# Kernel tuning notes

Hardware: AMD Instinct MI355X
Metric: run time of the kernel (lower is better)

## Reference

```python
import jax, jax.numpy as jnp
import numpy as np

N_HEADS = 16
N_KV_HEADS = 4
ROPE_BASE = 10000.0


def rotate_half(x):
    d = x.shape[-1] // 2
    return jnp.concatenate((-x[..., d:], x[..., :d]), axis=-1)


def rope_cos_sin(seq_len, head_dim, dtype):
    inv_freq = 1.0 / (ROPE_BASE ** (jnp.arange(0, head_dim, 2, dtype=jnp.float32) / head_dim))
    t = jnp.arange(seq_len, dtype=jnp.float32)
    freqs = jnp.outer(t, inv_freq)            # [S, d/2]
    emb = jnp.concatenate((freqs, freqs), axis=-1)  # [S, d]
    return emb.astype(dtype), None  # placeholder; cos/sin computed by caller


def setup_inputs() -> dict:
    key = jax.random.key(0)
    ks = jax.random.split(key, 5)
    B, S, H = 1, 2048, 2048
    kv_dim = (H // N_HEADS) * N_KV_HEADS  # 512
    scale = 1.0 / np.sqrt(H)
    return {
        "hidden_states": jax.random.normal(ks[0], (B, S, H), dtype=jnp.float32),
        "Wq": jax.random.normal(ks[1], (H, H), dtype=jnp.float32) * scale,
        "Wk": jax.random.normal(ks[2], (kv_dim, H), dtype=jnp.float32) * scale,
        "Wv": jax.random.normal(ks[3], (kv_dim, H), dtype=jnp.float32) * scale,
        "Wo": jax.random.normal(ks[4], (H, H), dtype=jnp.float32) * scale,
    }


def reference(hidden_states, Wq, Wk, Wv, Wo):
    B, S, H = hidden_states.shape
    nH, nKV = N_HEADS, N_KV_HEADS
    d = H // nH
    groups = nH // nKV

    # projections (nn.Linear: y = x @ W.T)
    q = (hidden_states @ Wq.T).reshape(B, S, nH, d)   # [B,S,nH,d]
    k = (hidden_states @ Wk.T).reshape(B, S, nKV, d)  # [B,S,nKV,d]
    v = (hidden_states @ Wv.T).reshape(B, S, nKV, d)

    # RoPE
    inv_freq = 1.0 / (ROPE_BASE ** (jnp.arange(0, d, 2, dtype=jnp.float32) / d))
    freqs = jnp.outer(jnp.arange(S, dtype=jnp.float32), inv_freq)  # [S,d/2]
    emb = jnp.concatenate((freqs, freqs), axis=-1)                 # [S,d]
    cos = jnp.cos(emb)[None, :, None, :]
    sin = jnp.sin(emb)[None, :, None, :]
    q = q * cos + rotate_half(q) * sin
    k = k * cos + rotate_half(k) * sin

    # GQA: repeat_interleave kv heads over head axis
    k = jnp.repeat(k, groups, axis=2)  # [B,S,nH,d]
    v = jnp.repeat(v, groups, axis=2)

    # causal scaled dot-product attention
    scores = jnp.einsum('bqhd,bkhd->bhqk', q, k) / jnp.sqrt(jnp.asarray(d, q.dtype))
    causal = jnp.tril(jnp.ones((S, S), dtype=bool))
    scores = jnp.where(causal[None, None], scores, jnp.asarray(-jnp.inf, scores.dtype))
    probs = jax.nn.softmax(scores, axis=-1)
    out = jnp.einsum('bhqk,bkhd->bqhd', probs, v)  # [B,S,nH,d]
    out = out.reshape(B, S, H) @ Wo.T
    return out
```

## Files before the change

kernel.cpp:

```cpp
#include <hip/hip_runtime.h>
#include <cstdint>
#include <cstddef>


typedef __bf16 bf16_t;
typedef bf16_t bf16x4_t __attribute__((ext_vector_type(4)));
typedef bf16_t bf16x8_t __attribute__((ext_vector_type(8)));
typedef float f32x4_t __attribute__((ext_vector_type(4)));

__device__ __forceinline__ void async_copy16(void* lds_base, const void* gsrc) {
  auto g = reinterpret_cast<__attribute__((address_space(1))) void*>(
      reinterpret_cast<uintptr_t>(gsrc));
  auto l = reinterpret_cast<__attribute__((address_space(3))) void*>(
      static_cast<uint32_t>(reinterpret_cast<uintptr_t>(lds_base)));
  __builtin_amdgcn_global_load_lds(g, l, 16, 0, 0);
}

__global__ __launch_bounds__(256) void cvt_all(const float* __restrict__ hs,
                                               const float* __restrict__ wq,
                                               const float* __restrict__ wk,
                                               const float* __restrict__ wv,
                                               const float* __restrict__ wo,
                                               bf16_t* __restrict__ regA,
                                               bf16_t* __restrict__ regB,
                                               bf16_t* __restrict__ regWo) {
  const int b = blockIdx.x;
  const float* src;
  bf16_t* dst;
  int rel;
  if (b < 2048) { src = hs; dst = regA; rel = b; }
  else if (b < 4096) { src = wq; dst = regB; rel = b - 2048; }
  else if (b < 4608) { src = wk; dst = regB + 4194304; rel = b - 4096; }
  else if (b < 5120) { src = wv; dst = regB + 5242880; rel = b - 4608; }
  else { src = wo; dst = regWo; rel = b - 5120; }
  const int i = (rel * 256 + threadIdx.x) * 8;
  float4 v0 = *(const float4*)(src + i);
  float4 v1 = *(const float4*)(src + i + 4);
  bf16x8_t o = {(bf16_t)v0.x, (bf16_t)v0.y, (bf16_t)v0.z, (bf16_t)v0.w,
                (bf16_t)v1.x, (bf16_t)v1.y, (bf16_t)v1.z, (bf16_t)v1.w};
  *(bf16x8_t*)(dst + i) = o;
}

template <typename OutT, bool ROPE>
__global__ __launch_bounds__(256) void gemm_bt64(const bf16_t* __restrict__ A,
                                                 const bf16_t* __restrict__ B,
                                                 OutT* __restrict__ C,
                                                 int M, int N, int K) {
  __shared__ bf16_t As[64 * 64];
  __shared__ bf16_t Bs[128 * 64];
  const int tid = threadIdx.x;
  const int lane = tid & 63;
  const int quad = lane >> 4;
  const int l15 = lane & 15;
  const int l7 = l15 & 7;
  const int wave = tid >> 6;
  const int bm = blockIdx.x * 64;
  const int bn = blockIdx.y * 128;
  const int wm = (wave >> 1) * 32;
  const int wn32 = (wave & 1) * 32;
  const int coff[4] = {wn32, wn32 + 16, wn32 + 64, wn32 + 80};

  f32x4_t acc[2][4] = {};

  for (int k0 = 0; k0 < K; k0 += 64) {
#pragma unroll
    for (int it = 0; it < 2; ++it) {
      const int slot = it * 256 + tid;
      const int r = slot >> 3;
      const int q = (slot & 7) ^ (r & 7);
      const int wbase = it * 2048 + (tid & 192) * 8;
      async_copy16(As + wbase, A + (size_t)(bm + r) * K + k0 + q * 8);
    }
#pragma unroll
    for (int it = 0; it < 4; ++it) {
      const int slot = it * 256 + tid;
      const int r = slot >> 3;
      const int q = (slot & 7) ^ (r & 7);
      const int wbase = it * 2048 + (tid & 192) * 8;
      async_copy16(Bs + wbase, B + (size_t)(bn + r) * K + k0 + q * 8);
    }
    __syncthreads();
#pragma unroll
    for (int kk = 0; kk < 64; kk += 32) {
      const int kc = kk >> 3;
      bf16x8_t af[2], bfv[4];
#pragma unroll
      for (int i = 0; i < 2; ++i)
        af[i] = *(const bf16x8_t*)(As + (wm + i * 16 + l15) * 64 +
                                   (((kc + quad) ^ l7) * 8));
#pragma unroll
      for (int i = 0; i < 4; ++i)
        bfv[i] = *(const bf16x8_t*)(Bs + (coff[i] + l15) * 64 +
                                    (((kc + quad) ^ l7) * 8));
#pragma unroll
      for (int mi = 0; mi < 2; ++mi)
#pragma unroll
        for (int ni = 0; ni < 4; ++ni)
          acc[mi][ni] = __builtin_amdgcn_mfma_f32_16x16x32_bf16(
              af[mi], bfv[ni], acc[mi][ni], 0, 0, 0);
    }
    __syncthreads();
  }

  if (ROPE && bn < 2560) {
#pragma unroll
    for (int pair = 0; pair < 2; ++pair) {
      const int i_d = wn32 + pair * 16 + l15;
      const float inv = exp2f(-(float)i_d * 0.20762050593045702f);
#pragma unroll
      for (int mi = 0; mi < 2; ++mi) {
#pragma unroll
        for (int r = 0; r < 4; ++r) {
          const int s_row = bm + wm + mi * 16 + quad * 4 + r;
          float sn, cs;
          sincosf((float)s_row * inv, &sn, &cs);
          const float x0 = acc[mi][pair][r];
          const float x1 = acc[mi][pair + 2][r];
          acc[mi][pair][r] = x0 * cs - x1 * sn;
          acc[mi][pair + 2][r] = x1 * cs + x0 * sn;
        }
      }
    }
  }

#pragma unroll
  for (int mi = 0; mi < 2; ++mi) {
#pragma unroll
    for (int r = 0; r < 4; ++r) {
      const int row = bm + wm + mi * 16 + quad * 4 + r;
#pragma unroll
      for (int ni = 0; ni < 4; ++ni)
        C[(size_t)row * N + bn + coff[ni] + l15] = (OutT)acc[mi][ni][r];
    }
  }
}

__global__ __launch_bounds__(256) void attn_kernel(
    const bf16_t* __restrict__ qkv, float* __restrict__ Op,
    float* __restrict__ lp) {
  __shared__ bf16_t Ks[64 * 128];
  __shared__ bf16_t Vt[128 * 64];
  __shared__ bf16_t Ps[4 * 16 * 64];
  const int tid = threadIdx.x;
  const int lane = tid & 63;
  const int wave = tid >> 6;
  const int quad = lane >> 4;
  const int l15 = lane & 15;
  const int l7 = l15 & 7;
  const int j = blockIdx.x;
  const int half = j >> 9;
  const int j2 = j & 511;
  const int qb = (j2 < 256) ? (31 - (j2 >> 4)) : ((j2 - 256) >> 4);
  const int h = j2 & 15;
  const int kvh = h >> 2;
  const int nh0 = (qb + 2) >> 1;
  const int kbS = half ? nh0 : 0;
  const int kbE = half ? (qb + 1) : nh0;
  const float scale = 0.08838834764831845f;

  const int rk0 = tid >> 4;
  const int cq = tid & 15;
  const int dv2 = lane * 2;

  bf16x8_t qf[4];
  {
    const bf16_t* qbase =
        qkv + (size_t)(qb * 64 + wave * 16 + l15) * 3072 + h * 128 + quad * 8;
#pragma unroll
    for (int kf = 0; kf < 4; ++kf) qf[kf] = *(const bf16x8_t*)(qbase + kf * 32);
  }

  f32x4_t o[8] = {};
  float lsum[4] = {0.f, 0.f, 0.f, 0.f};

  bf16x8_t kreg[4];
  uint32_t vbuf[2][8];
  auto load_tile = [&](int kb) {
    const bf16_t* kbase = qkv + (size_t)(kb * 64) * 3072 + 2048 + kvh * 128;
    const bf16_t* vbase = qkv + (size_t)(kb * 64) * 3072 + 2560 + kvh * 128;
#pragma unroll
    for (int it = 0; it < 4; ++it)
      kreg[it] =
          *(const bf16x8_t*)(kbase + (size_t)(it * 16 + rk0) * 3072 + cq * 8);
#pragma unroll
    for (int it = 0; it < 2; ++it) {
      const int kg8 = it * 4 + wave;
#pragma unroll
      for (int t = 0; t < 8; ++t)
        vbuf[it][t] =
            *(const uint32_t*)(vbase + (size_t)(kg8 * 8 + t) * 3072 + dv2);
    }
  };

  if (kbS < kbE) {
    load_tile(kbS);

    for (int kb = kbS; kb < kbE; ++kb) {
      __syncthreads();
#pragma unroll
      for (int it = 0; it < 4; ++it)
        *(bf16x8_t*)(Ks + (it * 16 + rk0) * 128 + ((cq ^ rk0) * 8)) = kreg[it];
#pragma unroll
      for (int it = 0; it < 2; ++it) {
        const int kg8 = it * 4 + wave;
        bf16x8_t lov, hiv;
#pragma unroll
        for (int t = 0; t < 8; ++t) {
          const uint32_t u = vbuf[it][t];
          lov[t] = __builtin_bit_cast(bf16_t, (unsigned short)(u & 0xffff));
          hiv[t] = __builtin_bit_cast(bf16_t, (unsigned short)(u >> 16));
        }
        *(bf16x8_t*)(Vt + (size_t)dv2 * 64 + ((kg8 ^ (dv2 & 7)) * 8)) = lov;
        *(bf16x8_t*)(Vt + (size_t)(dv2 + 1) * 64 +
                     ((kg8 ^ ((dv2 + 1) & 7)) * 8)) = hiv;
      }
      __syncthreads();
      if (kb + 1 < kbE) load_tile(kb + 1);

      f32x4_t sc[4] = {};
#pragma unroll
      for (int kf = 0; kf < 4; ++kf) {
#pragma unroll
        for (int ni = 0; ni < 4; ++ni) {
          bf16x8_t bfr = *(const bf16x8_t*)(Ks + (ni * 16 + l15) * 128 +
                                            (((kf * 4 + quad) ^ l15) * 8));
          sc[ni] = __builtin_amdgcn_mfma_f32_16x16x32_bf16(qf[kf], bfr, sc[ni],
                                                           0, 0, 0);
        }
      }

      float p[4][4];
#pragma unroll
      for (int r = 0; r < 4; ++r) {
        const int sq = qb * 64 + wave * 16 + quad * 4 + r;
#pragma unroll
        for (int ni = 0; ni < 4; ++ni) {
          float arg = fmaf(sc[ni][r], scale, -16.0f);
          if (kb == qb && (kb * 64 + ni * 16 + l15) > sq) arg = -100.0f;
          const float e = __expf(arg);
          p[ni][r] = e;
          lsum[r] += e;
        }
      }

      bf16_t* pw = Ps + wave * 16 * 64;
#pragma unroll
      for (int ni = 0; ni < 4; ++ni)
#pragma unroll
        for (int r = 0; r < 4; ++r) {
          const int prow = quad * 4 + r;
          pw[prow * 64 + (((ni * 2 + (l15 >> 3)) ^ (prow & 7)) * 8) + l7] =
              (bf16_t)p[ni][r];
        }

#pragma unroll
      for (int kf = 0; kf < 2; ++kf) {
        bf16x8_t af =
            *(const bf16x8_t*)(pw + l15 * 64 + (((kf * 4 + quad) ^ l7) * 8));
#pragma unroll
        for (int ni = 0; ni < 8; ++ni) {
          bf16x8_t bfr = *(const bf16x8_t*)(Vt + (ni * 16 + l15) * 64 +
                                            (((kf * 4 + quad) ^ l7) * 8));
          o[ni] =
              __builtin_amdgcn_mfma_f32_16x16x32_bf16(af, bfr, o[ni], 0, 0, 0);
        }
      }
    }
  }

#pragma unroll
  for (int m = 1; m <= 8; m <<= 1)
#pragma unroll
    for (int r = 0; r < 4; ++r) lsum[r] += __shfl_xor(lsum[r], m, 64);

  float* obase = Op + (size_t)half * 4194304 +
                 (size_t)(qb * 64 + wave * 16 + quad * 4) * 2048 + h * 128 + l15;
#pragma unroll
  for (int r = 0; r < 4; ++r) {
#pragma unroll
    for (int ni = 0; ni < 8; ++ni)
      obase[(size_t)r * 2048 + ni * 16] = o[ni][r];
    if (l15 == 0) {
      const int row = qb * 64 + wave * 16 + quad * 4 + r;
      lp[(half * 2048 + row) * 16 + h] = lsum[r];
    }
  }
}

__global__ __launch_bounds__(256) void combine_kernel(
    const float* __restrict__ Op, const float* __restrict__ lp,
    bf16_t* __restrict__ out) {
  const int idx = (blockIdx.x * 256 + threadIdx.x) * 8;
  const int s = idx >> 11;
  const int col = idx & 2047;
  const int h = col >> 7;
  const float l = lp[s * 16 + h] + lp[(2048 + s) * 16 + h];
  const float inv = 1.0f / l;
  const float* pa = Op + (size_t)s * 2048 + col;
  const float* pb = pa + 4194304;
  float4 a0 = *(const float4*)(pa);
  float4 a1 = *(const float4*)(pa + 4);
  float4 b0 = *(const float4*)(pb);
  float4 b1 = *(const float4*)(pb + 4);
  bf16x8_t o = {(bf16_t)((a0.x + b0.x) * inv), (bf16_t)((a0.y + b0.y) * inv),
                (bf16_t)((a0.z + b0.z) * inv), (bf16_t)((a0.w + b0.w) * inv),
                (bf16_t)((a1.x + b1.x) * inv), (bf16_t)((a1.y + b1.y) * inv),
                (bf16_t)((a1.z + b1.z) * inv), (bf16_t)((a1.w + b1.w) * inv)};
  *(bf16x8_t*)(out + idx) = o;
}

extern "C" void kernel_launch(void* const* d_in, const int* in_sizes, int n_in,
                              void* d_out, int out_size, void* d_ws, size_t ws_size,
                              hipStream_t stream) {
  const float* hidden = (const float*)d_in[0];
  const float* Wq = (const float*)d_in[1];
  const float* Wk = (const float*)d_in[2];
  const float* Wv = (const float*)d_in[3];
  const float* Wo = (const float*)d_in[4];

  char* ws = (char*)d_ws;
  bf16_t* regA = (bf16_t*)ws;
  bf16_t* regB = (bf16_t*)(ws + (size_t)(8u << 20));
  float* Opart = (float*)(ws + (size_t)(8u << 20));
  bf16_t* regC = (bf16_t*)(ws + (size_t)(40u << 20));
  bf16_t* regWo = (bf16_t*)(ws + (size_t)(53u << 20));
  float* lpart = (float*)(ws + (size_t)(61u << 20));

  cvt_all<<<7168, 256, 0, stream>>>(hidden, Wq, Wk, Wv, Wo, regA, regB, regWo);

  gemm_bt64<bf16_t, true><<<dim3(32, 24), 256, 0, stream>>>(regA, regB, regC,
                                                            2048, 3072, 2048);

  attn_kernel<<<1024, 256, 0, stream>>>(regC, Opart, lpart);

  combine_kernel<<<2048, 256, 0, stream>>>(Opart, lpart, regA);

  gemm_bt64<float, false><<<dim3(32, 16), 256, 0, stream>>>(
      regA, regWo, (float*)d_out, 2048, 2048, 2048);
}
```

Before: 218.0 us.

## Split attention KV range into variable segments per query block and reduce with atomics

```diff
diff --git a/kernel.cpp b/kernel.cpp
--- a/kernel.cpp
+++ b/kernel.cpp
@@ -14,6 +14,20 @@
   auto l = reinterpret_cast<__attribute__((address_space(3))) void*>(
       static_cast<uint32_t>(reinterpret_cast<uintptr_t>(lds_base)));
   __builtin_amdgcn_global_load_lds(g, l, 16, 0, 0);
+}
+
+__global__ __launch_bounds__(256) void zero_acc(float* __restrict__ Oacc,
+                                                float* __restrict__ lacc) {
+  const int i = (blockIdx.x * 256 + threadIdx.x) * 8;
+  float4 z = {0.f, 0.f, 0.f, 0.f};
+  if (i < 4194304) {
+    *(float4*)(Oacc + i) = z;
+    *(float4*)(Oacc + i + 4) = z;
+  } else {
+    const int k = i - 4194304;
+    *(float4*)(lacc + k) = z;
+    *(float4*)(lacc + k + 4) = z;
+  }
 }
 
 __global__ __launch_bounds__(256) void cvt_all(const float* __restrict__ hs,
@@ -136,8 +150,8 @@
 }
 
 __global__ __launch_bounds__(256) void attn_kernel(
-    const bf16_t* __restrict__ qkv, float* __restrict__ Op,
-    float* __restrict__ lp) {
+    const bf16_t* __restrict__ qkv, float* __restrict__ Oacc,
+    float* __restrict__ lacc) {
   __shared__ bf16_t Ks[64 * 128];
   __shared__ bf16_t Vt[128 * 64];
   __shared__ bf16_t Ps[4 * 16 * 64];
@@ -147,15 +161,24 @@
   const int quad = lane >> 4;
   const int l15 = lane & 15;
   const int l7 = l15 & 7;
-  const int j = blockIdx.x;
-  const int half = j >> 9;
-  const int j2 = j & 511;
-  const int qb = (j2 < 256) ? (31 - (j2 >> 4)) : ((j2 - 256) >> 4);
-  const int h = j2 & 15;
+  const int b = blockIdx.x;
+  const int h = b & 15;
+  const int w = b >> 4;
+  int qb, ns, seg;
+  if (w < 32) {
+    qb = 31 - (w >> 2); ns = 4; seg = w & 3;
+  } else if (w < 56) {
+    const int u = w - 32; qb = 23 - u / 3; ns = 3; seg = u % 3;
+  } else if (w < 72) {
+    const int u = w - 56; qb = 15 - (u >> 1); ns = 2; seg = u & 1;
+  } else {
+    qb = 7 - (w - 72); ns = 1; seg = 0;
+  }
+  const int T = qb + 1;
+  const int qd = T / ns, rem = T % ns;
+  const int kbS = seg * qd + (seg < rem ? seg : rem);
+  const int kbE = kbS + qd + (seg < rem ? 1 : 0);
   const int kvh = h >> 2;
-  const int nh0 = (qb + 2) >> 1;
-  const int kbS = half ? nh0 : 0;
-  const int kbE = half ? (qb + 1) : nh0;
   const float scale = 0.08838834764831845f;
 
   const int rk0 = tid >> 4;
@@ -192,7 +215,7 @@
     }
   };
 
-  if (kbS < kbE) {
+  {
     load_tile(kbS);
 
     for (int kb = kbS; kb < kbE; ++kb) {
@@ -273,39 +296,34 @@
 #pragma unroll
     for (int r = 0; r < 4; ++r) lsum[r] += __shfl_xor(lsum[r], m, 64);
 
-  float* obase = Op + (size_t)half * 4194304 +
-                 (size_t)(qb * 64 + wave * 16 + quad * 4) * 2048 + h * 128 + l15;
+  float* obase =
+      Oacc + (size_t)(qb * 64 + wave * 16 + quad * 4) * 2048 + h * 128 + l15;
 #pragma unroll
   for (int r = 0; r < 4; ++r) {
 #pragma unroll
     for (int ni = 0; ni < 8; ++ni)
-      obase[(size_t)r * 2048 + ni * 16] = o[ni][r];
+      atomicAdd(obase + (size_t)r * 2048 + ni * 16, o[ni][r]);
     if (l15 == 0) {
       const int row = qb * 64 + wave * 16 + quad * 4 + r;
-      lp[(half * 2048 + row) * 16 + h] = lsum[r];
+      atomicAdd(lacc + row * 16 + h, lsum[r]);
     }
   }
 }
 
 __global__ __launch_bounds__(256) void combine_kernel(
-    const float* __restrict__ Op, const float* __restrict__ lp,
+    const float* __restrict__ Oacc, const float* __restrict__ lacc,
     bf16_t* __restrict__ out) {
   const int idx = (blockIdx.x * 256 + threadIdx.x) * 8;
   const int s = idx >> 11;
   const int col = idx & 2047;
   const int h = col >> 7;
-  const float l = lp[s * 16 + h] + lp[(2048 + s) * 16 + h];
-  const float inv = 1.0f / l;
-  const float* pa = Op + (size_t)s * 2048 + col;
-  const float* pb = pa + 4194304;
-  float4 a0 = *(const float4*)(pa);
-  float4 a1 = *(const float4*)(pa + 4);
-  float4 b0 = *(const float4*)(pb);
-  float4 b1 = *(const float4*)(pb + 4);
-  bf16x8_t o = {(bf16_t)((a0.x + b0.x) * inv), (bf16_t)((a0.y + b0.y) * inv),
-                (bf16_t)((a0.z + b0.z) * inv), (bf16_t)((a0.w + b0.w) * inv),
-                (bf16_t)((a1.x + b1.x) * inv), (bf16_t)((a1.y + b1.y) * inv),
-                (bf16_t)((a1.z + b1.z) * inv), (bf16_t)((a1.w + b1.w) * inv)};
+  const float inv = 1.0f / lacc[s * 16 + h];
+  float4 a0 = *(const float4*)(Oacc + idx);
+  float4 a1 = *(const float4*)(Oacc + idx + 4);
+  bf16x8_t o = {(bf16_t)(a0.x * inv), (bf16_t)(a0.y * inv),
+                (bf16_t)(a0.z * inv), (bf16_t)(a0.w * inv),
+                (bf16_t)(a1.x * inv), (bf16_t)(a1.y * inv),
+                (bf16_t)(a1.z * inv), (bf16_t)(a1.w * inv)};
   *(bf16x8_t*)(out + idx) = o;
 }
 
@@ -321,19 +339,21 @@
   char* ws = (char*)d_ws;
   bf16_t* regA = (bf16_t*)ws;
   bf16_t* regB = (bf16_t*)(ws + (size_t)(8u << 20));
-  float* Opart = (float*)(ws + (size_t)(8u << 20));
+  float* Oacc = (float*)(ws + (size_t)(22u << 20));
+  float* lacc = (float*)(ws + (size_t)(39u << 20));
   bf16_t* regC = (bf16_t*)(ws + (size_t)(40u << 20));
   bf16_t* regWo = (bf16_t*)(ws + (size_t)(53u << 20));
-  float* lpart = (float*)(ws + (size_t)(61u << 20));
+
+  zero_acc<<<2064, 256, 0, stream>>>(Oacc, lacc);
 
   cvt_all<<<7168, 256, 0, stream>>>(hidden, Wq, Wk, Wv, Wo, regA, regB, regWo);
 
   gemm_bt64<bf16_t, true><<<dim3(32, 24), 256, 0, stream>>>(regA, regB, regC,
                                                             2048, 3072, 2048);
 
-  attn_kernel<<<1024, 256, 0, stream>>>(regC, Opart, lpart);
-
-  combine_kernel<<<2048, 256, 0, stream>>>(Opart, lpart, regA);
+  attn_kernel<<<1280, 256, 0, stream>>>(regC, Oacc, lacc);
+
+  combine_kernel<<<2048, 256, 0, stream>>>(Oacc, lacc, regA);
 
   gemm_bt64<float, false><<<dim3(32, 16), 256, 0, stream>>>(
       regA, regWo, (float*)d_out, 2048, 2048, 2048);
```

New measurement: 244.6 us. 1.12x slower.
